# Kernel optimization log

Hardware: AMD Instinct MI355X
Metric: run time of the kernel (lower is better)

Reference implementation:

```python
import jax, jax.numpy as jnp
import numpy as np

R = 2            # radix
N = 1024         # input_size (power of R)
DEPTH = 10       # log_R(N) levels
SIZES = [N >> l for l in range(DEPTH)]                 # per-level input_size: 1024,512,...,2
OFFSETS = np.concatenate([[0], np.cumsum(SIZES)])      # offsets into flat butterfly-weight vector
TOTAL_W = int(OFFSETS[-1])                             # 2046
# residual cascade in the torch code: int(True)-1 = 0 (False), int(0)-1 = -1 -> bool(-1)=True,
# and it stays truthy for all deeper levels.
RES = [True, False] + [True] * (DEPTH - 2)


def setup_inputs() -> dict:
    key = jax.random.key(0)
    k1, k2, k3 = jax.random.split(key, 3)
    x = jax.random.normal(k1, (4, 4096, N), dtype=jnp.float32)
    bw = jax.random.normal(k2, (TOTAL_W,), dtype=jnp.float32) * 0.1   # xavier-ish scale
    lw = jax.random.normal(k3, (DEPTH, R, R), dtype=jnp.float32) * 0.5
    return {"x": x, "bw": bw, "lw": lw}


def _fft(x, bw, lw, level):
    """One DIT radix-R butterfly level applied to the last dim of x (eval mode: dropout = id)."""
    n = x.shape[-1]                                   # input_size at this level
    o = int(OFFSETS[level])
    w = bw[o:o + n].reshape(R, n // R)                # elementwise 'twiddle' weights (r, n/r)
    xr = x.reshape(x.shape[:-1] + (R, n // R))        # (..., r, n/r)
    inner = _fft(xr, bw, lw, level + 1) if n > R else xr   # recurse on last dim n/r; Identity at base
    # torch: einsum('ij,...ik->...jk', lin_weights, weights * recursive(x))
    y = jnp.einsum('ij,...ik->...jk', lw[level], w * inner).reshape(x.shape)
    return x + y if RES[level] else y


def reference(x, bw, lw):
    return _fft(x, bw, lw, 0)
```

## Files before the change

### kernel.cpp

```cpp
#include <hip/hip_runtime.h>


constexpr int VECLEN = 1024;

__device__ __forceinline__ int swz(int f) {
  return f ^ (((f >> 5) & 7) << 2);
}

template<int L, bool RESL>
__device__ __forceinline__ void level_inlane(float (&v)[16], const float (&xr)[16],
                                             const float* __restrict__ bw,
                                             const float* __restrict__ lw) {
  constexpr int n = VECLEN >> L;
  constexpr int h = n >> 1;
  constexpr int off = 2048 - (2048 >> L);
  float w[n];
#pragma unroll
  for (int i = 0; i < n; ++i) w[i] = bw[off + i];
  const float l00 = lw[L*4+0], l01 = lw[L*4+1], l10 = lw[L*4+2], l11 = lw[L*4+3];
#pragma unroll
  for (int r = 0; r < 16; ++r) {
    if ((r & h) == 0) {
      const int q = r ^ h;
      const float t0 = w[r & (n-1)] * v[r];
      const float t1 = w[q & (n-1)] * v[q];
      const float y0 = l00*t0 + l10*t1;
      const float y1 = l01*t0 + l11*t1;
      v[r] = RESL ? xr[r] + y0 : y0;
      v[q] = RESL ? xr[q] + y1 : y1;
    }
  }
}

template<int L, bool RESL>
__device__ __forceinline__ void level_dpp(float (&v)[16], const float (&xr)[16],
                                          const float (&w)[16],
                                          const float* __restrict__ lw, int lane) {
  static_assert(L == 4 || L == 5, "DPP levels only");
  constexpr int ctl = (L == 5) ? 0xB1 : 0x4E;
  const int role = (lane >> (5 - L)) & 1;
  const float l00 = lw[L*4+0], l01 = lw[L*4+1], l10 = lw[L*4+2], l11 = lw[L*4+3];
  const float cs = role ? l11 : l00;
  const float cp = role ? l01 : l10;
#pragma unroll
  for (int r = 0; r < 16; ++r) {
    const float t = w[r] * v[r];
    const float tp = __int_as_float(
        __builtin_amdgcn_update_dpp(0, __float_as_int(t), ctl, 0xF, 0xF, true));
    const float y = cs*t + cp*tp;
    v[r] = RESL ? xr[r] + y : y;
  }
}

template<int L>
__device__ __forceinline__ void loadw_A(float (&w)[16], const float* lds_bw, int lane) {
  constexpr int n = VECLEN >> L;
  constexpr int off = 2048 - (2048 >> L);
  const int f0 = off + ((lane * 16) & (n - 1));
#pragma unroll
  for (int k = 0; k < 4; ++k) {
    const float4 f = *reinterpret_cast<const float4*>(lds_bw + swz(f0 + 4*k));
    w[4*k+0]=f.x; w[4*k+1]=f.y; w[4*k+2]=f.z; w[4*k+3]=f.w;
  }
}

template<int L>
__device__ __forceinline__ void loadw_B(float* w, const float* lds_bw, int lane) {
  constexpr int off = 2048 - (2048 >> L);
  constexpr int nr = (VECLEN >> L) >> 6;
#pragma unroll
  for (int j = 0; j < nr; ++j)
    w[j] = lds_bw[swz(off + j*64 + lane)];
}

template<int L, bool RESL>
__device__ __forceinline__ void level_B(float (&v)[16], const float (&xr)[16],
                                        const float* w, const float* __restrict__ lw) {
  constexpr int nr = (VECLEN >> L) >> 6;
  constexpr int hb = nr >> 1;
  const float l00 = lw[L*4+0], l01 = lw[L*4+1], l10 = lw[L*4+2], l11 = lw[L*4+3];
#pragma unroll
  for (int r = 0; r < 16; ++r) {
    if ((r & hb) == 0) {
      const int q = r ^ hb;
      const float t0 = w[r & (nr-1)] * v[r];
      const float t1 = w[q & (nr-1)] * v[q];
      const float y0 = l00*t0 + l10*t1;
      const float y1 = l01*t0 + l11*t1;
      v[r] = RESL ? xr[r] + y0 : y0;
      v[q] = RESL ? xr[q] + y1 : y1;
    }
  }
}

__device__ __forceinline__ void phaseA(float (&v)[16], const float (&xrA)[16],
                                       const float* lds_bw,
                                       const float* __restrict__ bw,
                                       const float* __restrict__ lw, int lane) {
  float wA[16], wB[16];
  loadw_A<5>(wA, lds_bw, lane);
  loadw_A<4>(wB, lds_bw, lane);
  level_inlane<9, true>(v, xrA, bw, lw);
  level_inlane<8, true>(v, xrA, bw, lw);
  level_inlane<7, true>(v, xrA, bw, lw);
  level_inlane<6, true>(v, xrA, bw, lw);
  level_dpp<5, true>(v, xrA, wA, lw, lane);
  level_dpp<4, true>(v, xrA, wB, lw, lane);
}

__device__ __forceinline__ void phaseB(float (&v)[16], const float (&xrB)[16],
                                       const float* lds_bw,
                                       const float* __restrict__ lw, int lane) {
  float w3[2], w2[4], w1[8], w0[16];
  loadw_B<3>(w3, lds_bw, lane);
  loadw_B<2>(w2, lds_bw, lane);
  level_B<3, true >(v, xrB, w3, lw);
  loadw_B<1>(w1, lds_bw, lane);
  level_B<2, true >(v, xrB, w2, lw);
  loadw_B<0>(w0, lds_bw, lane);
  level_B<1, false>(v, xrB, w1, lw);
  level_B<0, true >(v, xrB, w0, lw);
}

__device__ __forceinline__ void loadX_A(float (&xr)[16], const float* __restrict__ x,
                                        size_t base, int lane) {
#pragma unroll
  for (int k = 0; k < 4; ++k) {
    const float4 f = *reinterpret_cast<const float4*>(x + base + lane*16 + 4*k);
    xr[4*k+0]=f.x; xr[4*k+1]=f.y; xr[4*k+2]=f.z; xr[4*k+3]=f.w;
  }
}

__device__ __forceinline__ void loadX_B(float (&xr)[16], const float* __restrict__ x,
                                        size_t base, int lane) {
#pragma unroll
  for (int r = 0; r < 16; ++r) xr[r] = x[base + r*64 + lane];
}

__global__ __launch_bounds__(256)
__attribute__((amdgpu_waves_per_eu(3)))
void rnnfft_kernel(const float* __restrict__ x,
                   const float* __restrict__ bw,
                   const float* __restrict__ lw,
                   float* __restrict__ out, int nvec) {
  __shared__ float lds_bw[2048];
  __shared__ float tbuf[4][1024];
  const int t = threadIdx.x;
  const int w4 = t >> 6;
  const int lane = t & 63;
  const int wid = blockIdx.x * 4 + w4;
  const size_t baseA = (size_t)(2 * wid) * VECLEN;
  const size_t baseB = baseA + VECLEN;
  float* buf = tbuf[w4];

  float v[16], xrA[16], xrB[16];
  loadX_A(xrA, x, baseA, lane);
  loadX_B(xrB, x, baseA, lane);

  if (t < 252) {
    const float4 a = *reinterpret_cast<const float4*>(bw + 8*t);
    const float4 b = *reinterpret_cast<const float4*>(bw + 8*t + 4);
    *reinterpret_cast<float4*>(lds_bw + swz(8*t)) = a;
    *reinterpret_cast<float4*>(lds_bw + swz(8*t+4)) = b;
  }
  __syncthreads();

#pragma unroll
  for (int r = 0; r < 16; ++r) v[r] = xrA[r];
  phaseA(v, xrA, lds_bw, bw, lw, lane);

#pragma unroll
  for (int k = 0; k < 4; ++k) {
    float4 f;
    f.x = v[4*k+0]; f.y = v[4*k+1]; f.z = v[4*k+2]; f.w = v[4*k+3];
    *reinterpret_cast<float4*>(buf + swz(lane*16 + 4*k)) = f;
  }
  loadX_A(xrA, x, baseB, lane);

#pragma unroll
  for (int r = 0; r < 16; ++r) v[r] = buf[swz(r*64 + lane)];
  phaseB(v, xrB, lds_bw, lw, lane);
#pragma unroll
  for (int r = 0; r < 16; ++r) out[baseA + r*64 + lane] = v[r];

  loadX_B(xrB, x, baseB, lane);

#pragma unroll
  for (int r = 0; r < 16; ++r) v[r] = xrA[r];
  phaseA(v, xrA, lds_bw, bw, lw, lane);

#pragma unroll
  for (int k = 0; k < 4; ++k) {
    float4 f;
    f.x = v[4*k+0]; f.y = v[4*k+1]; f.z = v[4*k+2]; f.w = v[4*k+3];
    *reinterpret_cast<float4*>(buf + swz(lane*16 + 4*k)) = f;
  }
#pragma unroll
  for (int r = 0; r < 16; ++r) v[r] = buf[swz(r*64 + lane)];
  phaseB(v, xrB, lds_bw, lw, lane);
#pragma unroll
  for (int r = 0; r < 16; ++r) out[baseB + r*64 + lane] = v[r];
}

extern "C" void kernel_launch(void* const* d_in, const int* in_sizes, int n_in,
                              void* d_out, int out_size, void* d_ws, size_t ws_size,
                              hipStream_t stream) {
  const float* x  = (const float*)d_in[0];
  const float* bw = (const float*)d_in[1];
  const float* lw = (const float*)d_in[2];
  float* out = (float*)d_out;
  const int nvec = in_sizes[0] / VECLEN;
  const int nwave = nvec / 2;
  const int wpb = 4;
  const int blocks = (nwave + wpb - 1) / wpb;
  rnnfft_kernel<<<blocks, 256, 0, stream>>>(x, bw, lw, out, nvec);
}
```

Measured before the change: 31.12 us.

## Interleave two vectors' butterfly levels per wave and share twiddle loads

Each wave now runs phase A for both of its vectors side by side, level by level, then transposes both through LDS and runs phase B for both together. The goal is more instruction-level parallelism between two independent dependency chains, and loading phase-B twiddles once for both vectors. Because both vectors are live at once, register pressure roughly doubles, and the occupancy hint is relaxed to allow 2 to 4 waves per EU. The residual loads for phase B are now issued later, just before the transposes, instead of overlapping phase A compute as before.

```diff
diff --git a/kernel.cpp b/kernel.cpp
--- a/kernel.cpp
+++ b/kernel.cpp
@@ -93,35 +93,6 @@
   }
 }
 
-__device__ __forceinline__ void phaseA(float (&v)[16], const float (&xrA)[16],
-                                       const float* lds_bw,
-                                       const float* __restrict__ bw,
-                                       const float* __restrict__ lw, int lane) {
-  float wA[16], wB[16];
-  loadw_A<5>(wA, lds_bw, lane);
-  loadw_A<4>(wB, lds_bw, lane);
-  level_inlane<9, true>(v, xrA, bw, lw);
-  level_inlane<8, true>(v, xrA, bw, lw);
-  level_inlane<7, true>(v, xrA, bw, lw);
-  level_inlane<6, true>(v, xrA, bw, lw);
-  level_dpp<5, true>(v, xrA, wA, lw, lane);
-  level_dpp<4, true>(v, xrA, wB, lw, lane);
-}
-
-__device__ __forceinline__ void phaseB(float (&v)[16], const float (&xrB)[16],
-                                       const float* lds_bw,
-                                       const float* __restrict__ lw, int lane) {
-  float w3[2], w2[4], w1[8], w0[16];
-  loadw_B<3>(w3, lds_bw, lane);
-  loadw_B<2>(w2, lds_bw, lane);
-  level_B<3, true >(v, xrB, w3, lw);
-  loadw_B<1>(w1, lds_bw, lane);
-  level_B<2, true >(v, xrB, w2, lw);
-  loadw_B<0>(w0, lds_bw, lane);
-  level_B<1, false>(v, xrB, w1, lw);
-  level_B<0, true >(v, xrB, w0, lw);
-}
-
 __device__ __forceinline__ void loadX_A(float (&xr)[16], const float* __restrict__ x,
                                         size_t base, int lane) {
 #pragma unroll
@@ -138,7 +109,7 @@
 }
 
 __global__ __launch_bounds__(256)
-__attribute__((amdgpu_waves_per_eu(3)))
+__attribute__((amdgpu_waves_per_eu(2, 4)))
 void rnnfft_kernel(const float* __restrict__ x,
                    const float* __restrict__ bw,
                    const float* __restrict__ lw,
@@ -153,9 +124,9 @@
   const size_t baseB = baseA + VECLEN;
   float* buf = tbuf[w4];
 
-  float v[16], xrA[16], xrB[16];
-  loadX_A(xrA, x, baseA, lane);
-  loadX_B(xrB, x, baseA, lane);
+  float vA[16], vB[16], xr0[16], xr1[16];
+  loadX_A(xr0, x, baseA, lane);
+  loadX_A(xr1, x, baseB, lane);
 
   if (t < 252) {
     const float4 a = *reinterpret_cast<const float4*>(bw + 8*t);
@@ -166,40 +137,55 @@
   __syncthreads();
 
 #pragma unroll
-  for (int r = 0; r < 16; ++r) v[r] = xrA[r];
-  phaseA(v, xrA, lds_bw, bw, lw, lane);
+  for (int r = 0; r < 16; ++r) { vA[r] = xr0[r]; vB[r] = xr1[r]; }
+
+  {
+    float wA[16], wB[16];
+    loadw_A<5>(wA, lds_bw, lane);
+    loadw_A<4>(wB, lds_bw, lane);
+    level_inlane<9, true>(vA, xr0, bw, lw);  level_inlane<9, true>(vB, xr1, bw, lw);
+    level_inlane<8, true>(vA, xr0, bw, lw);  level_inlane<8, true>(vB, xr1, bw, lw);
+    level_inlane<7, true>(vA, xr0, bw, lw);  level_inlane<7, true>(vB, xr1, bw, lw);
+    level_inlane<6, true>(vA, xr0, bw, lw);  level_inlane<6, true>(vB, xr1, bw, lw);
+    level_dpp<5, true>(vA, xr0, wA, lw, lane); level_dpp<5, true>(vB, xr1, wA, lw, lane);
+    level_dpp<4, true>(vA, xr0, wB, lw, lane); level_dpp<4, true>(vB, xr1, wB, lw, lane);
+  }
 
 #pragma unroll
   for (int k = 0; k < 4; ++k) {
     float4 f;
-    f.x = v[4*k+0]; f.y = v[4*k+1]; f.z = v[4*k+2]; f.w = v[4*k+3];
+    f.x = vA[4*k+0]; f.y = vA[4*k+1]; f.z = vA[4*k+2]; f.w = vA[4*k+3];
     *reinterpret_cast<float4*>(buf + swz(lane*16 + 4*k)) = f;
   }
-  loadX_A(xrA, x, baseB, lane);
-
-#pragma unroll
-  for (int r = 0; r < 16; ++r) v[r] = buf[swz(r*64 + lane)];
-  phaseB(v, xrB, lds_bw, lw, lane);
-#pragma unroll
-  for (int r = 0; r < 16; ++r) out[baseA + r*64 + lane] = v[r];
-
-  loadX_B(xrB, x, baseB, lane);
-
-#pragma unroll
-  for (int r = 0; r < 16; ++r) v[r] = xrA[r];
-  phaseA(v, xrA, lds_bw, bw, lw, lane);
-
+  loadX_B(xr0, x, baseA, lane);
+#pragma unroll
+  for (int r = 0; r < 16; ++r) vA[r] = buf[swz(r*64 + lane)];
 #pragma unroll
   for (int k = 0; k < 4; ++k) {
     float4 f;
-    f.x = v[4*k+0]; f.y = v[4*k+1]; f.z = v[4*k+2]; f.w = v[4*k+3];
+    f.x = vB[4*k+0]; f.y = vB[4*k+1]; f.z = vB[4*k+2]; f.w = vB[4*k+3];
     *reinterpret_cast<float4*>(buf + swz(lane*16 + 4*k)) = f;
   }
-#pragma unroll
-  for (int r = 0; r < 16; ++r) v[r] = buf[swz(r*64 + lane)];
-  phaseB(v, xrB, lds_bw, lw, lane);
-#pragma unroll
-  for (int r = 0; r < 16; ++r) out[baseB + r*64 + lane] = v[r];
+  loadX_B(xr1, x, baseB, lane);
+#pragma unroll
+  for (int r = 0; r < 16; ++r) vB[r] = buf[swz(r*64 + lane)];
+
+  {
+    float w3[2], w2[4], w1[8], w0[16];
+    loadw_B<3>(w3, lds_bw, lane);
+    loadw_B<2>(w2, lds_bw, lane);
+    loadw_B<1>(w1, lds_bw, lane);
+    loadw_B<0>(w0, lds_bw, lane);
+    level_B<3, true >(vA, xr0, w3, lw);  level_B<3, true >(vB, xr1, w3, lw);
+    level_B<2, true >(vA, xr0, w2, lw);  level_B<2, true >(vB, xr1, w2, lw);
+    level_B<1, false>(vA, xr0, w1, lw);  level_B<1, false>(vB, xr1, w1, lw);
+    level_B<0, true >(vA, xr0, w0, lw);  level_B<0, true >(vB, xr1, w0, lw);
+  }
+
+#pragma unroll
+  for (int r = 0; r < 16; ++r) out[baseA + r*64 + lane] = vA[r];
+#pragma unroll
+  for (int r = 0; r < 16; ++r) out[baseB + r*64 + lane] = vB[r];
 }
 
 extern "C" void kernel_launch(void* const* d_in, const int* in_sizes, int n_in,
```

After: 37.73 us. +21.3%, slower.
